# Performance work log

Measured on AMD Instinct MI355X. Metric: run time of the kernel, lower is better.

The kernel has to match this reference:

```python
import jax, jax.numpy as jnp
import numpy as np

SPARSITY = 0.9

def setup_inputs() -> dict:
    key = jax.random.key(0)
    k1, k2, k3 = jax.random.split(key, 3)
    B, IN, OUT = 8192, 4096, 4096
    x = jax.random.normal(k1, (B, IN), dtype=jnp.float32)
    weight = jax.random.normal(k2, (OUT, IN), dtype=jnp.float32)
    mask = jax.random.uniform(k3, (OUT, IN)) > SPARSITY
    weight = weight * mask.astype(jnp.float32)  # pre-masked, like weight.to_sparse()
    bias = jnp.zeros((OUT,), dtype=jnp.float32)
    return {"x": x, "weight": weight, "bias": bias, "mask": mask}

def reference(x, weight, bias, mask):
    # out = (W_sparse @ x.T).T + b  ==  x @ W.T + b with W zero off-pattern
    w = weight * mask.astype(weight.dtype)
    out = jnp.einsum('bi,oi->bo', x, w) + bias  # [B, OUT]
    return out
```

## Files before the change

### kernel.cpp

```cpp
#include <hip/hip_runtime.h>
#include <hip/hip_bf16.h>

#define M_DIM 8192
#define N_DIM 4096
#define K_DIM 4096

using bf16x8 = __attribute__((ext_vector_type(8))) short;
using f32x4  = __attribute__((ext_vector_type(4))) float;

__device__ __forceinline__ unsigned short f2bf(float f) {
    unsigned int u = __float_as_uint(f);
    unsigned int r = u + 0x7fffu + ((u >> 16) & 1u);
    return (unsigned short)(r >> 16);
}

__global__ void cvt_both_f32_to_bf16(const float* __restrict__ x,
                                     const float* __restrict__ w,
                                     unsigned short* __restrict__ ws,
                                     int n4x, int n4w) {
    int i = blockIdx.x * blockDim.x + threadIdx.x;
    const int stride = gridDim.x * blockDim.x;
    const int total = n4x + n4w;
    uint2* dx = reinterpret_cast<uint2*>(ws);
    uint2* dw = reinterpret_cast<uint2*>(ws) + n4x;
    for (; i < total; i += stride) {
        const bool isX = i < n4x;
        const float4* s4 = isX ? reinterpret_cast<const float4*>(x)
                               : reinterpret_cast<const float4*>(w);
        const int j = isX ? i : i - n4x;
        float4 v = s4[j];
        uint2 o;
        o.x = (unsigned)f2bf(v.x) | ((unsigned)f2bf(v.y) << 16);
        o.y = (unsigned)f2bf(v.z) | ((unsigned)f2bf(v.w) << 16);
        (isX ? dx : dw)[j] = o;
    }
}

__device__ __forceinline__ void gload16(const unsigned short* g, char* l) {
    __builtin_amdgcn_global_load_lds(
        (const __attribute__((address_space(1))) void*)g,
        (__attribute__((address_space(3))) void*)l, 16, 0, 0);
}

__global__ __launch_bounds__(512, 2) void gemm_bf16_256_8ph(
        const unsigned short* __restrict__ xb,
        const unsigned short* __restrict__ wb,
        const float* __restrict__ bias,
        float* __restrict__ out) {
    extern __shared__ char lds[];
    char* ldsA = lds;
    char* ldsB = lds + 65536;

    const int bid = blockIdx.x;
    const int xcd = bid & 7;
    const int c   = bid >> 3;
    const int tm  = (xcd >> 1) * 8 + (c & 7);
    const int tn  = (xcd & 1) * 8 + (c >> 3);
    const int r0 = tm * 256;
    const int c0 = tn * 256;

    const int tid  = threadIdx.x;
    const int lane = tid & 63;
    const int wave = tid >> 6;
    const int wm = wave >> 2;
    const int wn = wave & 3;
    const int lr = lane & 15;
    const int t4 = lane >> 4;

    int aRd[4][2], bRd[2][2];
    const int swz = (lr & 7) << 4;
#pragma unroll
    for (int ks = 0; ks < 2; ++ks) {
        const int cb = (ks * 64 + t4 * 16) ^ swz;
#pragma unroll
        for (int m = 0; m < 4; ++m)
            aRd[m][ks] = (wm * 64 + m * 16 + lr) * 128 + cb;
#pragma unroll
        for (int n = 0; n < 2; ++n)
            bRd[n][ks] = (wn * 32 + n * 16 + lr) * 128 + cb;
    }

    const int rowInBlk = lane >> 3;
    const int sChunk   = ((lane & 7) ^ rowInBlk) * 8;
    int aSrcB[2], bSrcB[2], dstOff[2];
#pragma unroll
    for (int l = 0; l < 2; ++l) {
        const int R0 = wave * 16 + l * 8;
        aSrcB[l] = (r0 + (R0 >> 6) * 128 + (R0 & 63) + rowInBlk) * K_DIM + sChunk;
        bSrcB[l] = (c0 + (R0 >> 5) * 64  + (R0 & 31) + rowInBlk) * K_DIM + sChunk;
        dstOff[l] = R0 * 128;
    }

    auto STAGE_A = [&](int q, int kt, int nb) {
#pragma unroll
        for (int l = 0; l < 2; ++l)
            gload16(xb + aSrcB[l] + q * 64 * K_DIM + kt * 64,
                    ldsA + nb * 32768 + q * 16384 + dstOff[l]);
    };
    auto STAGE_B = [&](int p, int kt, int nb) {
#pragma unroll
        for (int l = 0; l < 2; ++l)
            gload16(wb + bSrcB[l] + p * 32 * K_DIM + kt * 64,
                    ldsB + nb * 32768 + p * 16384 + dstOff[l]);
    };

    f32x4 acc[8][4];
#pragma unroll
    for (int i = 0; i < 8; ++i)
#pragma unroll
        for (int j = 0; j < 4; ++j)
            acc[i][j] = (f32x4){0.f, 0.f, 0.f, 0.f};

    bf16x8 av[4][2], bvA[2][2], bvB[2][2], bv1[2][2];

#define MFMA_QUAD(M0, N0, BV)                                                  \
    do {                                                                       \
        __builtin_amdgcn_s_setprio(1);                                         \
        _Pragma("unroll") for (int m = 0; m < 4; ++m)                          \
        _Pragma("unroll") for (int n = 0; n < 2; ++n)                          \
        _Pragma("unroll") for (int ks = 0; ks < 2; ++ks)                       \
            acc[(M0) + m][(N0) + n] = __builtin_amdgcn_mfma_f32_16x16x32_bf16( \
                av[m][ks], BV[n][ks], acc[(M0) + m][(N0) + n], 0, 0, 0);       \
        __builtin_amdgcn_s_setprio(0);                                         \
    } while (0)

#define LOAD_A(Q, BUF)                                                         \
    _Pragma("unroll") for (int m = 0; m < 4; ++m)                              \
    _Pragma("unroll") for (int ks = 0; ks < 2; ++ks)                           \
        av[m][ks] = *(const bf16x8*)(ldsA + (BUF) * 32768 + (Q) * 16384 + aRd[m][ks]);

#define LOAD_B(P, BUF, BV)                                                     \
    _Pragma("unroll") for (int n = 0; n < 2; ++n)                              \
    _Pragma("unroll") for (int ks = 0; ks < 2; ++ks)                           \
        BV[n][ks] = *(const bf16x8*)(ldsB + (BUF) * 32768 + (P) * 16384 + bRd[n][ks]);

    const int NT = K_DIM / 64;

#define TILE_BODY(T, BUF, XV, YV)                                              \
    do {                                                                       \
        const int nb_  = (BUF) ^ 1;                                           \
        const int kt1_ = ((T) + 1) & (NT - 1);                                 \
        const int kt2_ = ((T) + 2) & (NT - 1);                                 \
                                      \
        STAGE_A(1, kt1_, nb_);                                                 \
        LOAD_B(1, (BUF), bv1);                                                 \
        MFMA_QUAD(0, 0, XV);                                                   \
        asm volatile("s_barrier" ::: "memory");                                \
                   \
        STAGE_A(0, kt2_, (BUF));                                               \
        MFMA_QUAD(0, 2, bv1);                                                  \
        LOAD_A(1, (BUF));                                                      \
        asm volatile("s_waitcnt vmcnt(6)\n\ts_barrier" ::: "memory");          \
                               \
        STAGE_B(0, kt2_, (BUF));                                               \
        LOAD_B(0, nb_, YV);                                                    \
        MFMA_QUAD(4, 2, bv1);                                                  \
        asm volatile("s_barrier" ::: "memory");                                \
                   \
        STAGE_B(1, kt2_, (BUF));                                               \
        MFMA_QUAD(4, 0, XV);                                                   \
        LOAD_A(0, nb_);                                                        \
        asm volatile("s_waitcnt vmcnt(6)\n\ts_barrier" ::: "memory");          \
    } while (0)

    STAGE_A(0, 0, 0);
    STAGE_B(0, 0, 0);
    STAGE_B(1, 0, 0);
    STAGE_A(1, 0, 0);
    STAGE_A(0, 1, 1);
    STAGE_B(0, 1, 1);
    STAGE_B(1, 1, 1);
    asm volatile("s_waitcnt vmcnt(6)\n\ts_barrier" ::: "memory");
    LOAD_A(0, 0);
    LOAD_B(0, 0, bvA);

    for (int tt = 0; tt < NT / 2; ++tt) {
        TILE_BODY(2 * tt,     0, bvA, bvB);
        TILE_BODY(2 * tt + 1, 1, bvB, bvA);
    }
    asm volatile("s_waitcnt vmcnt(0)" ::: "memory");

#pragma unroll
    for (int ni = 0; ni < 4; ++ni) {
        const int col = c0 + wn * 64 + (ni >> 1) * 32 + (ni & 1) * 16 + lr;
        const float bvs = bias[col];
#pragma unroll
        for (int mi = 0; mi < 8; ++mi) {
            const int row0 = r0 + wm * 128 + (mi >> 2) * 64 + (mi & 3) * 16 + t4 * 4;
#pragma unroll
            for (int j = 0; j < 4; ++j)
                out[(row0 + j) * N_DIM + col] = acc[mi][ni][j] + bvs;
        }
    }
#undef TILE_BODY
#undef MFMA_QUAD
#undef LOAD_A
#undef LOAD_B
}

__global__ __launch_bounds__(256) void gemm_bf16_mfma(
        const unsigned short* __restrict__ xb,
        const unsigned short* __restrict__ wb,
        const float* __restrict__ bias,
        float* __restrict__ out) {
    __shared__ unsigned short sA[128 * 64];
    __shared__ unsigned short sB[128 * 64];

    const int nwg = (M_DIM / 128) * (N_DIM / 128);
    const int q = nwg / 8;
    int bid = blockIdx.x;
    int bid2 = (bid & 7) * q + (bid >> 3);
    const int tm = bid2 & 63;
    const int tn = bid2 >> 6;
    const int r0 = tm * 128;
    const int c0 = tn * 128;

    const int tid  = threadIdx.x;
    const int lane = tid & 63;
    const int wave = tid >> 6;
    const int wr = wave >> 1;
    const int wc = wave & 1;
    const int lr = lane & 15;
    const int t  = lane >> 4;

    int aoff[2][4], boff[2][4];
#pragma unroll
    for (int m = 0; m < 4; ++m) {
        int rowA = wr * 64 + m * 16 + lr;
        int swA  = (rowA & 7) << 4;
        int rowB = wc * 64 + m * 16 + lr;
        int swB  = (rowB & 7) << 4;
#pragma unroll
        for (int kk = 0; kk < 2; ++kk) {
            int cb = kk * 64 + t * 16;
            aoff[kk][m] = rowA * 64 + ((cb ^ swA) >> 1);
            boff[kk][m] = rowB * 64 + ((cb ^ swB) >> 1);
        }
    }

    const int sRow   = lane >> 3;
    const int sChunk = (lane & 7) ^ sRow;
    int aSrc[4], bSrc[4];
    char* ldsA[4];
    char* ldsB[4];
#pragma unroll
    for (int r = 0; r < 4; ++r) {
        int row = r * 32 + wave * 8 + sRow;
        aSrc[r] = (r0 + row) * K_DIM + sChunk * 8;
        bSrc[r] = (c0 + row) * K_DIM + sChunk * 8;
        ldsA[r] = (char*)sA + (r * 4 + wave) * 1024;
        ldsB[r] = (char*)sB + (r * 4 + wave) * 1024;
    }

    f32x4 acc[4][4];
#pragma unroll
    for (int m = 0; m < 4; ++m)
#pragma unroll
        for (int n = 0; n < 4; ++n)
            acc[m][n] = (f32x4){0.f, 0.f, 0.f, 0.f};

    for (int kt = 0; kt < K_DIM / 64; ++kt) {
        const int ko = kt * 64;
#pragma unroll
        for (int r = 0; r < 4; ++r) {
            gload16(xb + aSrc[r] + ko, ldsA[r]);
            gload16(wb + bSrc[r] + ko, ldsB[r]);
        }
        __syncthreads();
#pragma unroll
        for (int kk = 0; kk < 2; ++kk) {
            bf16x8 av[4], bv[4];
#pragma unroll
            for (int m = 0; m < 4; ++m)
                av[m] = *reinterpret_cast<const bf16x8*>(sA + aoff[kk][m]);
#pragma unroll
            for (int n = 0; n < 4; ++n)
                bv[n] = *reinterpret_cast<const bf16x8*>(sB + boff[kk][n]);
#pragma unroll
            for (int m = 0; m < 4; ++m)
#pragma unroll
                for (int n = 0; n < 4; ++n)
                    acc[m][n] = __builtin_amdgcn_mfma_f32_16x16x32_bf16(
                        av[m], bv[n], acc[m][n], 0, 0, 0);
        }
        __syncthreads();
    }

#pragma unroll
    for (int n = 0; n < 4; ++n) {
        const int col = c0 + wc * 64 + n * 16 + lr;
        const float bv = bias[col];
#pragma unroll
        for (int m = 0; m < 4; ++m) {
            const int row0 = r0 + wr * 64 + m * 16 + t * 4;
#pragma unroll
            for (int j = 0; j < 4; ++j)
                out[(row0 + j) * N_DIM + col] = acc[m][n][j] + bv;
        }
    }
}

__global__ void fallback_gemm_f32(const float* __restrict__ x,
                                  const float* __restrict__ w,
                                  const float* __restrict__ bias,
                                  float* __restrict__ out) {
    __shared__ float sX[2][4096];
    const int tid = threadIdx.x;
    const int col = blockIdx.x * 256 + tid;
    const int row0 = blockIdx.y * 2;
    for (int i = tid * 4; i < 8192; i += 1024) {
        int r = i >> 12, c = i & 4095;
        *(float4*)&sX[r][c] = *(const float4*)&x[(size_t)(row0 + r) * 4096 + c];
    }
    __syncthreads();
    const float4* wrow = (const float4*)&w[(size_t)col * 4096];
    float a0 = 0.f, a1 = 0.f;
    for (int k4 = 0; k4 < 1024; ++k4) {
        float4 wv = wrow[k4];
        int k = k4 << 2;
        a0 += wv.x * sX[0][k] + wv.y * sX[0][k + 1] + wv.z * sX[0][k + 2] + wv.w * sX[0][k + 3];
        a1 += wv.x * sX[1][k] + wv.y * sX[1][k + 1] + wv.z * sX[1][k + 2] + wv.w * sX[1][k + 3];
    }
    float bv = bias[col];
    out[(size_t)row0 * 4096 + col] = a0 + bv;
    out[(size_t)(row0 + 1) * 4096 + col] = a1 + bv;
}

extern "C" void kernel_launch(void* const* d_in, const int* in_sizes, int n_in,
                              void* d_out, int out_size, void* d_ws, size_t ws_size,
                              hipStream_t stream) {
    const float* x    = (const float*)d_in[0];
    const float* w    = (const float*)d_in[1];
    const float* bias = (const float*)d_in[2];
    float* out = (float*)d_out;

    const size_t nX = (size_t)M_DIM * K_DIM;
    const size_t nW = (size_t)N_DIM * K_DIM;
    const size_t need = (nX + nW) * sizeof(unsigned short);

    if (ws_size >= need) {
        unsigned short* xb = (unsigned short*)d_ws;
        unsigned short* wb = xb + nX;
        cvt_both_f32_to_bf16<<<3072, 256, 0, stream>>>(
            x, w, (unsigned short*)d_ws, (int)(nX / 4), (int)(nW / 4));
        hipError_t e = hipFuncSetAttribute(
            (const void*)gemm_bf16_256_8ph,
            hipFuncAttributeMaxDynamicSharedMemorySize, 131072);
        if (e == hipSuccess) {
            gemm_bf16_256_8ph<<<(M_DIM / 256) * (N_DIM / 256), 512, 131072, stream>>>(
                xb, wb, bias, out);
        } else {
            gemm_bf16_mfma<<<(M_DIM / 128) * (N_DIM / 128), 256, 0, stream>>>(
                xb, wb, bias, out);
        }
    } else {
        fallback_gemm_f32<<<dim3(N_DIM / 256, M_DIM / 2), 256, 0, stream>>>(x, w, bias, out);
    }
}
```

Baseline: 260.8 us.

## Switch 256x256 GEMM tile from 8 waves to 4 waves with 128x128 per wave

Restructures the bf16 MFMA GEMM so each workgroup of 4 waves (256 threads) computes the 256x256 tile, with each wave owning a 128x128 sub-tile (8x8 MFMA accumulators) instead of 64x128 across 8 waves. Staging loads per wave double, the wait counts and phase ordering in the 4-phase pipeline are adjusted, and the LDS fragment reads are reindexed. The aim is more register-level reuse per LDS read and fewer waves contending at barriers. The risks are high VGPR/AGPR pressure (256 accumulator registers), reduced latency hiding from fewer waves, and possible spills.

```diff
diff --git a/kernel.cpp b/kernel.cpp
--- a/kernel.cpp
+++ b/kernel.cpp
@@ -42,7 +42,7 @@
         (__attribute__((address_space(3))) void*)l, 16, 0, 0);
 }
 
-__global__ __launch_bounds__(512, 2) void gemm_bf16_256_8ph(
+__global__ __launch_bounds__(256, 1) void gemm_bf16_256_w4(
         const unsigned short* __restrict__ xb,
         const unsigned short* __restrict__ wb,
         const float* __restrict__ bias,
@@ -62,77 +62,70 @@
     const int tid  = threadIdx.x;
     const int lane = tid & 63;
     const int wave = tid >> 6;
-    const int wm = wave >> 2;
-    const int wn = wave & 3;
+    const int wm = wave >> 1;
+    const int wn = wave & 1;
     const int lr = lane & 15;
     const int t4 = lane >> 4;
 
-    int aRd[4][2], bRd[2][2];
     const int swz = (lr & 7) << 4;
-#pragma unroll
-    for (int ks = 0; ks < 2; ++ks) {
-        const int cb = (ks * 64 + t4 * 16) ^ swz;
-#pragma unroll
-        for (int m = 0; m < 4; ++m)
-            aRd[m][ks] = (wm * 64 + m * 16 + lr) * 128 + cb;
-#pragma unroll
-        for (int n = 0; n < 2; ++n)
-            bRd[n][ks] = (wn * 32 + n * 16 + lr) * 128 + cb;
-    }
+    int cb[2];
+#pragma unroll
+    for (int ks = 0; ks < 2; ++ks)
+        cb[ks] = (ks * 64 + t4 * 16) ^ swz;
+    const int aBase = wm * 16384 + lr * 128;
+    const int bBase = wn * 16384 + lr * 128;
 
     const int rowInBlk = lane >> 3;
     const int sChunk   = ((lane & 7) ^ rowInBlk) * 8;
-    int aSrcB[2], bSrcB[2], dstOff[2];
-#pragma unroll
-    for (int l = 0; l < 2; ++l) {
-        const int R0 = wave * 16 + l * 8;
-        aSrcB[l] = (r0 + (R0 >> 6) * 128 + (R0 & 63) + rowInBlk) * K_DIM + sChunk;
-        bSrcB[l] = (c0 + (R0 >> 5) * 64  + (R0 & 31) + rowInBlk) * K_DIM + sChunk;
-        dstOff[l] = R0 * 128;
-    }
 
     auto STAGE_A = [&](int q, int kt, int nb) {
 #pragma unroll
-        for (int l = 0; l < 2; ++l)
-            gload16(xb + aSrcB[l] + q * 64 * K_DIM + kt * 64,
-                    ldsA + nb * 32768 + q * 16384 + dstOff[l]);
+        for (int l = 0; l < 4; ++l)
+            gload16(xb + (r0 + q * 128 + wave * 32 + l * 8 + rowInBlk) * K_DIM
+                       + sChunk + kt * 64,
+                    ldsA + nb * 32768 + q * 16384 + wave * 4096 + l * 1024);
     };
     auto STAGE_B = [&](int p, int kt, int nb) {
 #pragma unroll
-        for (int l = 0; l < 2; ++l)
-            gload16(wb + bSrcB[l] + p * 32 * K_DIM + kt * 64,
-                    ldsB + nb * 32768 + p * 16384 + dstOff[l]);
+        for (int l = 0; l < 4; ++l)
+            gload16(wb + (c0 + p * 128 + wave * 32 + l * 8 + rowInBlk) * K_DIM
+                       + sChunk + kt * 64,
+                    ldsB + nb * 32768 + p * 16384 + wave * 4096 + l * 1024);
     };
 
-    f32x4 acc[8][4];
+    f32x4 acc[8][8];
 #pragma unroll
     for (int i = 0; i < 8; ++i)
 #pragma unroll
-        for (int j = 0; j < 4; ++j)
+        for (int j = 0; j < 8; ++j)
             acc[i][j] = (f32x4){0.f, 0.f, 0.f, 0.f};
 
-    bf16x8 av[4][2], bvA[2][2], bvB[2][2], bv1[2][2];
-
-#define MFMA_QUAD(M0, N0, BV)                                                  \
+    bf16x8 av[4][2], bvX[4][2], bvY[4][2], bv1[4][2];
+
+#define LOAD_AH(H, BUF)                                                        \
+    _Pragma("unroll") for (int m = 0; m < 4; ++m)                              \
+    _Pragma("unroll") for (int ks = 0; ks < 2; ++ks)                           \
+        av[m][ks] = *(const bf16x8*)(ldsA + (BUF) * 32768 + aBase              \
+                                     + ((H) * 4 + m) * 2048 + cb[ks]);
+
+#define LOAD_BH(H, BUF, BV)                                                    \
+    _Pragma("unroll") for (int n = 0; n < 4; ++n)                              \
+    _Pragma("unroll") for (int ks = 0; ks < 2; ++ks)                           \
+        (BV)[n][ks] = *(const bf16x8*)(ldsB + (BUF) * 32768 + bBase            \
+                                       + ((H) * 4 + n) * 2048 + cb[ks]);
+
+#define MFMA_QUAD(MH, NH, BV)                                                  \
     do {                                                                       \
         __builtin_amdgcn_s_setprio(1);                                         \
         _Pragma("unroll") for (int m = 0; m < 4; ++m)                          \
-        _Pragma("unroll") for (int n = 0; n < 2; ++n)                          \
+        _Pragma("unroll") for (int n = 0; n < 4; ++n)                          \
         _Pragma("unroll") for (int ks = 0; ks < 2; ++ks)                       \
-            acc[(M0) + m][(N0) + n] = __builtin_amdgcn_mfma_f32_16x16x32_bf16( \
-                av[m][ks], BV[n][ks], acc[(M0) + m][(N0) + n], 0, 0, 0);       \
+            acc[(MH) * 4 + m][(NH) * 4 + n] =                                  \
+                __builtin_amdgcn_mfma_f32_16x16x32_bf16(                       \
+                    av[m][ks], (BV)[n][ks], acc[(MH) * 4 + m][(NH) * 4 + n],   \
+                    0, 0, 0);                                                  \
         __builtin_amdgcn_s_setprio(0);                                         \
     } while (0)
-
-#define LOAD_A(Q, BUF)                                                         \
-    _Pragma("unroll") for (int m = 0; m < 4; ++m)                              \
-    _Pragma("unroll") for (int ks = 0; ks < 2; ++ks)                           \
-        av[m][ks] = *(const bf16x8*)(ldsA + (BUF) * 32768 + (Q) * 16384 + aRd[m][ks]);
-
-#define LOAD_B(P, BUF, BV)                                                     \
-    _Pragma("unroll") for (int n = 0; n < 2; ++n)                              \
-    _Pragma("unroll") for (int ks = 0; ks < 2; ++ks)                           \
-        BV[n][ks] = *(const bf16x8*)(ldsB + (BUF) * 32768 + (P) * 16384 + bRd[n][ks]);
 
     const int NT = K_DIM / 64;
 
@@ -141,52 +134,52 @@
         const int nb_  = (BUF) ^ 1;                                           \
         const int kt1_ = ((T) + 1) & (NT - 1);                                 \
         const int kt2_ = ((T) + 2) & (NT - 1);                                 \
-                                      \
+             \
         STAGE_A(1, kt1_, nb_);                                                 \
-        LOAD_B(1, (BUF), bv1);                                                 \
+        LOAD_BH(1, (BUF), bv1);                                                \
         MFMA_QUAD(0, 0, XV);                                                   \
-        asm volatile("s_barrier" ::: "memory");                                \
-                   \
+        asm volatile("s_waitcnt vmcnt(16)\n\ts_barrier" ::: "memory");         \
+              \
+        STAGE_B(0, kt2_, (BUF));                                               \
+        MFMA_QUAD(0, 1, bv1);                                                  \
+        LOAD_AH(1, (BUF));                                                     \
+        asm volatile("s_waitcnt vmcnt(16)\n\ts_barrier" ::: "memory");         \
+               \
         STAGE_A(0, kt2_, (BUF));                                               \
-        MFMA_QUAD(0, 2, bv1);                                                  \
-        LOAD_A(1, (BUF));                                                      \
-        asm volatile("s_waitcnt vmcnt(6)\n\ts_barrier" ::: "memory");          \
-                               \
-        STAGE_B(0, kt2_, (BUF));                                               \
-        LOAD_B(0, nb_, YV);                                                    \
-        MFMA_QUAD(4, 2, bv1);                                                  \
-        asm volatile("s_barrier" ::: "memory");                                \
-                   \
+        LOAD_BH(0, nb_, YV);                                                   \
+        MFMA_QUAD(1, 1, bv1);                                                  \
+        asm volatile("s_waitcnt vmcnt(8)\n\ts_barrier" ::: "memory");          \
+              \
         STAGE_B(1, kt2_, (BUF));                                               \
-        MFMA_QUAD(4, 0, XV);                                                   \
-        LOAD_A(0, nb_);                                                        \
-        asm volatile("s_waitcnt vmcnt(6)\n\ts_barrier" ::: "memory");          \
+        MFMA_QUAD(1, 0, XV);                                                   \
+        LOAD_AH(0, nb_);                                                       \
+        asm volatile("s_waitcnt vmcnt(16)\n\ts_barrier" ::: "memory");         \
     } while (0)
 
     STAGE_A(0, 0, 0);
+    STAGE_A(1, 0, 0);
     STAGE_B(0, 0, 0);
     STAGE_B(1, 0, 0);
-    STAGE_A(1, 0, 0);
     STAGE_A(0, 1, 1);
     STAGE_B(0, 1, 1);
     STAGE_B(1, 1, 1);
-    asm volatile("s_waitcnt vmcnt(6)\n\ts_barrier" ::: "memory");
-    LOAD_A(0, 0);
-    LOAD_B(0, 0, bvA);
+    asm volatile("s_waitcnt vmcnt(12)\n\ts_barrier" ::: "memory");
+    LOAD_AH(0, 0);
+    LOAD_BH(0, 0, bvX);
 
     for (int tt = 0; tt < NT / 2; ++tt) {
-        TILE_BODY(2 * tt,     0, bvA, bvB);
-        TILE_BODY(2 * tt + 1, 1, bvB, bvA);
+        TILE_BODY(2 * tt,     0, bvX, bvY);
+        TILE_BODY(2 * tt + 1, 1, bvY, bvX);
     }
     asm volatile("s_waitcnt vmcnt(0)" ::: "memory");
 
 #pragma unroll
-    for (int ni = 0; ni < 4; ++ni) {
-        const int col = c0 + wn * 64 + (ni >> 1) * 32 + (ni & 1) * 16 + lr;
+    for (int ni = 0; ni < 8; ++ni) {
+        const int col = c0 + wn * 128 + ni * 16 + lr;
         const float bvs = bias[col];
 #pragma unroll
         for (int mi = 0; mi < 8; ++mi) {
-            const int row0 = r0 + wm * 128 + (mi >> 2) * 64 + (mi & 3) * 16 + t4 * 4;
+            const int row0 = r0 + wm * 128 + mi * 16 + t4 * 4;
 #pragma unroll
             for (int j = 0; j < 4; ++j)
                 out[(row0 + j) * N_DIM + col] = acc[mi][ni][j] + bvs;
@@ -194,8 +187,8 @@
     }
 #undef TILE_BODY
 #undef MFMA_QUAD
-#undef LOAD_A
-#undef LOAD_B
+#undef LOAD_AH
+#undef LOAD_BH
 }
 
 __global__ __launch_bounds__(256) void gemm_bf16_mfma(
@@ -344,10 +337,10 @@
         cvt_both_f32_to_bf16<<<3072, 256, 0, stream>>>(
             x, w, (unsigned short*)d_ws, (int)(nX / 4), (int)(nW / 4));
         hipError_t e = hipFuncSetAttribute(
-            (const void*)gemm_bf16_256_8ph,
+            (const void*)gemm_bf16_256_w4,
             hipFuncAttributeMaxDynamicSharedMemorySize, 131072);
         if (e == hipSuccess) {
-            gemm_bf16_256_8ph<<<(M_DIM / 256) * (N_DIM / 256), 512, 131072, stream>>>(
+            gemm_bf16_256_w4<<<(M_DIM / 256) * (N_DIM / 256), 256, 131072, stream>>>(
                 xb, wb, bias, out);
         } else {
             gemm_bf16_mfma<<<(M_DIM / 128) * (N_DIM / 128), 256, 0, stream>>>(
```

Result: slower. 994.0 us (+281.1%).
